# Optimization experiments

Measured on AMD Instinct MI355X. Metric: run time of the kernel, lower is better.

## Reference

```python
import jax, jax.numpy as jnp
import numpy as np

N = 100_000      # nodes
E = 1_600_000    # edges (avg degree 16)
D_IN = 128
D_OUT = 128
K = 64           # low-rank attention rank


def setup_inputs() -> dict:
    key = jax.random.key(0)
    ks = jax.random.split(key, 6)
    s = lambda d: 1.0 / np.sqrt(d)
    return {
        "x": jax.random.normal(ks[0], (N, D_IN), dtype=jnp.float32),
        "edge_index": jax.random.randint(ks[1], (2, E), 0, N, dtype=jnp.int32),
        "W_gcn": jax.random.normal(ks[2], (D_IN, D_OUT), dtype=jnp.float32) * s(D_IN),
        "b_gcn": jnp.zeros((D_OUT,), jnp.float32),
        "W_att": jax.random.normal(ks[3], (D_IN, 4 * K), dtype=jnp.float32) * s(D_IN),
        "b_att": jnp.zeros((4 * K,), jnp.float32),
        "W_red": jax.random.normal(ks[4], (D_OUT + 2 * K, D_OUT), dtype=jnp.float32) * s(D_OUT + 2 * K),
        "b_red": jnp.zeros((D_OUT,), jnp.float32),
    }


def _forward(x, W_gcn, b_gcn, W_att, b_att, W_red, b_red, edge_index):
    n = x.shape[0]
    # --- GCN conv (symmetric normalization, self-loops), dropout = identity (eval) ---
    loop = jnp.arange(n, dtype=edge_index.dtype)
    src = jnp.concatenate([edge_index[0], loop])
    dst = jnp.concatenate([edge_index[1], loop])
    deg = jax.ops.segment_sum(jnp.ones_like(dst, dtype=x.dtype), dst, num_segments=n)
    dinv = jax.lax.rsqrt(deg)                      # deg >= 1 due to self-loops
    norm = dinv[src] * dinv[dst]                   # [E+n]
    h = x @ W_gcn                                  # [n, D_OUT]
    agg = jax.ops.segment_sum(h[src] * norm[:, None], dst, num_segments=n) + b_gcn
    x_local = jax.nn.relu(agg)

    # --- Low-rank global attention (LRGA) ---
    t = jax.nn.relu(x @ W_att + b_att)             # [n, 4K]
    U, V, Z, T = jnp.split(t, 4, axis=1)           # each [n, K]
    # joint_normalize2: scalar 1/mean(U @ (V^T @ 1_n))
    D = 1.0 / jnp.mean(U @ (V.T @ jnp.ones((n, 1), x.dtype)))
    res = (U @ (V.T @ Z)) * D                      # [n, K]
    x_global = jnp.concatenate([res, T], axis=1)   # [n, 2K]

    # --- fuse + dim reduce ---
    return jnp.concatenate([x_local, x_global], axis=1) @ W_red + b_red


def reference(x, edge_index, W_gcn, b_gcn, W_att, b_att, W_red, b_red):
    return _forward(x, W_gcn, b_gcn, W_att, b_att, W_red, b_red, edge_index)
```

## Files before the change

### kernel.cpp

```cpp
#include <hip/hip_runtime.h>

#define DIN   128
#define DOUT  128
#define KR    64
#define TCOLS 256
#define WCOLS 384
#define P_RED 1024
#define PSTR  4224

typedef unsigned short ushort_t;
typedef __attribute__((ext_vector_type(8))) short bf16x8;
typedef __attribute__((ext_vector_type(4))) float f32x4;

__device__ __forceinline__ float bf2f(unsigned short u) {
  return __uint_as_float(((unsigned int)u) << 16);
}
__device__ __forceinline__ unsigned short f2bf(float f) {
  unsigned int b = __float_as_uint(f);
  b = b + 0x7FFFu + ((b >> 16) & 1u);
  return (unsigned short)(b >> 16);
}

__global__ __launch_bounds__(256) void k_init(int* __restrict__ degc, float* __restrict__ VtZ,
                                              float* __restrict__ colsum, int* __restrict__ bcur,
                                              int N) {
  int i = blockIdx.x * 256 + threadIdx.x;
  if (i < N) degc[i] = 1;
  if (i < 4096) VtZ[i] = 0.f;
  if (i < 128) colsum[i] = 0.f;
  if (i < 128) bcur[i] = 0;
}

__global__ __launch_bounds__(256) void k_deg(const int* __restrict__ ei, int* __restrict__ degc, int E) {
  int e = blockIdx.x * 256 + threadIdx.x;
  if (e < E) atomicAdd(&degc[ei[E + e]], 1);
}

__global__ __launch_bounds__(256) void k_split(const float* __restrict__ x,
                                               ushort_t* __restrict__ xhF, ushort_t* __restrict__ xloF,
                                               int N, int total_slots) {
  int gid = blockIdx.x * 256 + threadIdx.x;
  int stride = gridDim.x * 256;
  for (; gid < total_slots; gid += stride) {
    int f = gid >> 6, l = gid & 63;
    int r16 = f >> 2, s = f & 3;
    int row = r16 * 16 + (l & 15);
    int k = s * 32 + ((l >> 4) << 3);
    ushort4 h0, h1, l0, l1;
    if (row < N) {
      float4 a = *(const float4*)&x[(size_t)row * DIN + k];
      float4 b = *(const float4*)&x[(size_t)row * DIN + k + 4];
      h0.x = f2bf(a.x); h0.y = f2bf(a.y); h0.z = f2bf(a.z); h0.w = f2bf(a.w);
      h1.x = f2bf(b.x); h1.y = f2bf(b.y); h1.z = f2bf(b.z); h1.w = f2bf(b.w);
      l0.x = f2bf(a.x - bf2f(h0.x)); l0.y = f2bf(a.y - bf2f(h0.y));
      l0.z = f2bf(a.z - bf2f(h0.z)); l0.w = f2bf(a.w - bf2f(h0.w));
      l1.x = f2bf(b.x - bf2f(h1.x)); l1.y = f2bf(b.y - bf2f(h1.y));
      l1.z = f2bf(b.z - bf2f(h1.z)); l1.w = f2bf(b.w - bf2f(h1.w));
    } else {
      h0 = make_ushort4(0, 0, 0, 0); h1 = h0; l0 = h0; l1 = h0;
    }
    ((ushort4*)xhF)[gid * 2] = h0;
    ((ushort4*)xhF)[gid * 2 + 1] = h1;
    ((ushort4*)xloF)[gid * 2] = l0;
    ((ushort4*)xloF)[gid * 2 + 1] = l1;
  }
}

__global__ __launch_bounds__(256) void k_wprep(const float* __restrict__ Wg, const float* __restrict__ Wa,
                                               ushort_t* __restrict__ whF, ushort_t* __restrict__ wlF) {
  int g = blockIdx.x * 256 + threadIdx.x;
  int f = g >> 6, l = g & 63;
  int c16 = f >> 2, s = f & 3;
  int col = c16 * 16 + (l & 15);
  int k = s * 32 + ((l >> 4) << 3);
#pragma unroll
  for (int j = 0; j < 8; ++j) {
    float v = (col < DOUT) ? Wg[(size_t)(k + j) * DOUT + col]
                           : Wa[(size_t)(k + j) * TCOLS + (col - DOUT)];
    ushort_t h = f2bf(v);
    whF[(size_t)g * 8 + j] = h;
    wlF[(size_t)g * 8 + j] = f2bf(v - bf2f(h));
  }
}

__global__ __launch_bounds__(256) void k_scan1(const int* __restrict__ degc, int* __restrict__ offs,
                                               int* __restrict__ bsums, int N) {
  __shared__ int s[256];
  int tid = threadIdx.x;
  int base = blockIdx.x * 1024 + tid * 4;
  int c[4], e[4];
#pragma unroll
  for (int q = 0; q < 4; ++q) c[q] = (base + q < N) ? (degc[base + q] - 1) : 0;
  e[0] = 0; e[1] = c[0]; e[2] = e[1] + c[1]; e[3] = e[2] + c[2];
  int tsum = e[3] + c[3];
  s[tid] = tsum; __syncthreads();
  for (int off = 1; off < 256; off <<= 1) {
    int v = (tid >= off) ? s[tid - off] : 0;
    __syncthreads();
    s[tid] += v;
    __syncthreads();
  }
  int tb = s[tid] - tsum;
#pragma unroll
  for (int q = 0; q < 4; ++q) if (base + q < N) offs[base + q] = tb + e[q];
  if (tid == 255) bsums[blockIdx.x] = s[255];
}

__global__ __launch_bounds__(128) void k_scan2(const int* __restrict__ bsums, int* __restrict__ boff,
                                               int* __restrict__ offs, int NBLK, int N) {
  __shared__ int s[128];
  int tid = threadIdx.x;
  int v = (tid < NBLK) ? bsums[tid] : 0;
  s[tid] = v; __syncthreads();
  for (int off = 1; off < 128; off <<= 1) {
    int u = (tid >= off) ? s[tid - off] : 0;
    __syncthreads();
    s[tid] += u;
    __syncthreads();
  }
  boff[tid] = s[tid] - v;
  if (tid == 127) offs[N] = s[127];
}

__global__ __launch_bounds__(256) void k_scan3(int* __restrict__ offs, const int* __restrict__ boff,
                                               const int* __restrict__ degc, float* __restrict__ dinv,
                                               int* __restrict__ cursor, int N) {
  int i = blockIdx.x * 256 + threadIdx.x;
  if (i < N) {
    offs[i] += boff[i >> 10];
    dinv[i] = rsqrtf((float)degc[i]);
    cursor[i] = 0;
  }
}

__global__ __launch_bounds__(256) void k_bin(const int* __restrict__ ei, int* __restrict__ bcur,
                                             int2* __restrict__ buckets, int* __restrict__ cursor,
                                             const int* __restrict__ offs, const float* __restrict__ dinv,
                                             int2* __restrict__ csr, int E, int B, int CAP) {
  __shared__ int hist[128], pref[128], place[128], gbase[128];
  __shared__ int2 st[4096];
  int tid = threadIdx.x;
  int e0 = blockIdx.x * 4096;
  int nE = min(4096, E - e0);
  if (nE <= 0) return;

  if (tid < 128) { hist[tid] = 0; place[tid] = 0; }
  __syncthreads();

  int src[16], dst[16];
#pragma unroll
  for (int q = 0; q < 16; ++q) {
    int idx = tid + q * 256;
    if (idx < nE) {
      src[q] = ei[e0 + idx];
      dst[q] = ei[E + e0 + idx];
      atomicAdd(&hist[dst[q] >> 10], 1);
    }
  }
  __syncthreads();

  if (tid < 128) pref[tid] = hist[tid];
  __syncthreads();
  for (int off = 1; off < 128; off <<= 1) {
    int v = (tid < 128 && tid >= off) ? pref[tid - off] : 0;
    __syncthreads();
    if (tid < 128) pref[tid] += v;
    __syncthreads();
  }
  if (tid < 128) pref[tid] -= hist[tid];
  if (tid < B && hist[tid] > 0) gbase[tid] = atomicAdd(&bcur[tid], hist[tid]);
  __syncthreads();

#pragma unroll
  for (int q = 0; q < 16; ++q) {
    int idx = tid + q * 256;
    if (idx < nE) {
      int b = dst[q] >> 10;
      int p = pref[b] + atomicAdd(&place[b], 1);
      st[p] = make_int2(src[q], dst[q]);
    }
  }
  __syncthreads();

  for (int i = tid; i < nE; i += 256) {
    int2 q = st[i];
    int b = q.y >> 10;
    int gp = gbase[b] + (i - pref[b]);
    if (gp < CAP) {
      buckets[(size_t)b * CAP + gp] = q;
    } else {
      int pos = atomicAdd(&cursor[q.y], 1);
      int2 c;
      c.x = q.x;
      c.y = __float_as_int(dinv[q.x] * dinv[q.y]);
      csr[offs[q.y] + pos] = c;
    }
  }
}

__global__ __launch_bounds__(256) void k_scatter2(const int2* __restrict__ buckets,
                                                  const int* __restrict__ bcur,
                                                  int* __restrict__ cursor, const int* __restrict__ offs,
                                                  const float* __restrict__ dinv,
                                                  int2* __restrict__ csr, int CAP) {
  int b = blockIdx.x;
  int n = min(bcur[b], CAP);
  const int2* sp = &buckets[(size_t)b * CAP];
  for (int i = threadIdx.x; i < n; i += 256) {
    int2 q = sp[i];
    int pos = atomicAdd(&cursor[q.y], 1);
    int2 c;
    c.x = q.x;
    c.y = __float_as_int(dinv[q.x] * dinv[q.y]);
    csr[offs[q.y] + pos] = c;
  }
}

#define LOADK(S, AH, AL, BH, BL)                                              \
  {                                                                           \
    _Pragma("unroll") for (int m_ = 0; m_ < 4; ++m_) {                        \
      size_t fo_ = (((size_t)(r16b + m_) * 4 + (S)) * 64 + lane) * 8;         \
      AH[m_] = *(const bf16x8*)&xhF[fo_];                                     \
      AL[m_] = *(const bf16x8*)&xloF[fo_];                                    \
    }                                                                         \
    _Pragma("unroll") for (int n_ = 0; n_ < 4; ++n_) {                        \
      size_t fo_ = (((size_t)(c16b + n_) * 4 + (S)) * 64 + lane) * 8;         \
      BH[n_] = *(const bf16x8*)&whF[fo_];                                     \
      BL[n_] = *(const bf16x8*)&wlF[fo_];                                     \
    }                                                                         \
  }

__global__ __launch_bounds__(256) void k_gemm1_mfma(const ushort_t* __restrict__ xhF,
                                                    const ushort_t* __restrict__ xloF,
                                                    const ushort_t* __restrict__ whF,
                                                    const ushort_t* __restrict__ wlF,
                                                    const float* __restrict__ ba,
                                                    ushort_t* __restrict__ hs, ushort_t* __restrict__ t,
                                                    int N, int ntiles) {
  int bid = blockIdx.x;
  int g = bid / 24;
  int rem = bid - g * 24;
  int colblk = rem >> 3;
  int ytile = g * 8 + (rem & 7);
  if (ytile >= ntiles) return;

  int tid = threadIdx.x;
  int lane = tid & 63;
  int wave = tid >> 6;
  int wr = wave >> 1, wc = wave & 1;
  int rowbase = ytile * 128 + wr * 64;
  int gcb = colblk * 128 + wc * 64;
  int r16b = ytile * 8 + wr * 4;
  int c16b = colblk * 8 + wc * 4;
  int lr = lane & 15;
  int rq = (lane >> 4) * 4;

  f32x4 acc[4][4] = {};
  bf16x8 ah[2][4], al[2][4], bh[2][4], bl[2][4];

  LOADK(0, ah[0], al[0], bh[0], bl[0]);
#pragma unroll
  for (int s = 0; s < 4; ++s) {
    int cur = s & 1, nxt = cur ^ 1;
    if (s < 3) LOADK(s + 1, ah[nxt], al[nxt], bh[nxt], bl[nxt]);
#pragma unroll
    for (int m = 0; m < 4; ++m)
#pragma unroll
      for (int n = 0; n < 4; ++n) {
        acc[m][n] = __builtin_amdgcn_mfma_f32_16x16x32_bf16(ah[cur][m], bl[cur][n], acc[m][n], 0, 0, 0);
        acc[m][n] = __builtin_amdgcn_mfma_f32_16x16x32_bf16(al[cur][m], bh[cur][n], acc[m][n], 0, 0, 0);
        acc[m][n] = __builtin_amdgcn_mfma_f32_16x16x32_bf16(ah[cur][m], bh[cur][n], acc[m][n], 0, 0, 0);
      }
  }

  if (colblk == 0) {
#pragma unroll
    for (int m = 0; m < 4; ++m)
#pragma unroll
      for (int i = 0; i < 4; ++i) {
        int row = rowbase + m * 16 + rq + i;
        if (row < N) {
#pragma unroll
          for (int n = 0; n < 4; ++n)
            hs[(size_t)row * DOUT + gcb + n * 16 + lr] = f2bf(acc[m][n][i]);
        }
      }
  } else {
    float bav[4];
#pragma unroll
    for (int n = 0; n < 4; ++n) bav[n] = ba[gcb - DOUT + n * 16 + lr];
#pragma unroll
    for (int m = 0; m < 4; ++m)
#pragma unroll
      for (int i = 0; i < 4; ++i) {
        int row = rowbase + m * 16 + rq + i;
        if (row < N) {
#pragma unroll
          for (int n = 0; n < 4; ++n)
            t[(size_t)row * TCOLS + gcb - DOUT + n * 16 + lr] =
                f2bf(fmaxf(acc[m][n][i] + bav[n], 0.f));
        }
      }
  }
}

__global__ __launch_bounds__(256) void k_red(const ushort_t* __restrict__ t, float* __restrict__ part,
                                             int N) {
  __shared__ float csh[512];
  int tid = threadIdx.x;
  int lane = tid & 63;
  int w = tid >> 6;
  int lr = lane & 15;
  int lk = (lane >> 4) * 8;
  int vcol = 64 + w * 16 + lr;
  int col2 = lane * 2;

  f32x4 acc[4] = {};
  float cs0 = 0.f, cs1 = 0.f;
  int ntiles = (N + 31) >> 5;

  for (int tile = blockIdx.x; tile < ntiles; tile += gridDim.x) {
    int r0 = tile * 32;
    const ushort_t* base = &t[(size_t)r0 * TCOLS];
    bf16x8 a, b[4];
    if (r0 + 32 <= N) {
#pragma unroll
      for (int j = 0; j < 8; ++j)
        ((short*)&a)[j] = (short)base[(size_t)(lk + j) * TCOLS + vcol];
#pragma unroll
      for (int n = 0; n < 4; ++n)
#pragma unroll
        for (int j = 0; j < 8; ++j)
          ((short*)&b[n])[j] = (short)base[(size_t)(lk + j) * TCOLS + 128 + n * 16 + lr];
#pragma unroll
      for (int j = 0; j < 8; ++j) {
        ushort2 u = *(const ushort2*)&base[(size_t)(w * 8 + j) * TCOLS + col2];
        cs0 += bf2f(u.x); cs1 += bf2f(u.y);
      }
    } else {
#pragma unroll
      for (int j = 0; j < 8; ++j) {
        int r = r0 + lk + j;
        ((short*)&a)[j] = (r < N) ? (short)t[(size_t)r * TCOLS + vcol] : (short)0;
      }
#pragma unroll
      for (int n = 0; n < 4; ++n)
#pragma unroll
        for (int j = 0; j < 8; ++j) {
          int r = r0 + lk + j;
          ((short*)&b[n])[j] = (r < N) ? (short)t[(size_t)r * TCOLS + 128 + n * 16 + lr] : (short)0;
        }
#pragma unroll
      for (int j = 0; j < 8; ++j) {
        int r = r0 + w * 8 + j;
        if (r < N) {
          ushort2 u = *(const ushort2*)&t[(size_t)r * TCOLS + col2];
          cs0 += bf2f(u.x); cs1 += bf2f(u.y);
        }
      }
    }
#pragma unroll
    for (int n = 0; n < 4; ++n)
      acc[n] = __builtin_amdgcn_mfma_f32_16x16x32_bf16(a, b[n], acc[n], 0, 0, 0);
  }

  float* pb = &part[(size_t)blockIdx.x * PSTR];
  int rq = (lane >> 4) * 4;
#pragma unroll
  for (int n = 0; n < 4; ++n)
#pragma unroll
    for (int i = 0; i < 4; ++i)
      pb[(w * 16 + rq + i) * 64 + n * 16 + lr] = acc[n][i];

  csh[tid] = cs0;
  csh[256 + tid] = cs1;
  __syncthreads();
  if (w == 0) {
    float t0 = csh[lane] + csh[64 + lane] + csh[128 + lane] + csh[192 + lane];
    float t1 = csh[256 + lane] + csh[320 + lane] + csh[384 + lane] + csh[448 + lane];
    pb[4096 + col2] = t0;
    pb[4096 + col2 + 1] = t1;
  }
}

__global__ __launch_bounds__(256) void k_redsum(const float* __restrict__ part,
                                                float* __restrict__ VtZ, float* __restrict__ colsum) {
  __shared__ float s[256];
  int tid = threadIdx.x;
  int j = blockIdx.x * 64 + (tid & 63);
  int bc = tid >> 6;
  float a = 0.f;
#pragma unroll 4
  for (int b = bc; b < P_RED; b += 4) a += part[(size_t)b * PSTR + j];
  s[tid] = a;
  __syncthreads();
  if (bc == 0) {
    float v = s[tid] + s[tid + 64] + s[tid + 128] + s[tid + 192];
    if (j < 4096) VtZ[j] = v;
    else colsum[j - 4096] = v;
  }
}

__global__ __launch_bounds__(64) void k_d(const float* __restrict__ colsum, float* __restrict__ Dws, int N) {
  __shared__ float s[64];
  int k = threadIdx.x;
  s[k] = colsum[k] * colsum[64 + k];
  __syncthreads();
  for (int off = 32; off > 0; off >>= 1) {
    if (k < off) s[k] += s[k + off];
    __syncthreads();
  }
  if (k == 0) {
    float p = s[0];
    Dws[0] = (p != 0.f) ? ((float)N / p) : 0.f;
  }
}

__global__ __launch_bounds__(256) void k_prep(const float* __restrict__ VtZ,
                                              const float* __restrict__ Dws,
                                              const float* __restrict__ Wr,
                                              ushort_t* __restrict__ weffT) {
  int c = blockIdx.x;
  int k = threadIdx.x;
  float v;
  if (k < 128 || k >= 192) {
    v = Wr[(size_t)k * DOUT + c];
  } else {
    float Dv = Dws[0];
    int kk = k - 128;
    float acc = 0.f;
#pragma unroll 8
    for (int j = 0; j < 64; ++j)
      acc += VtZ[kk * 64 + j] * Wr[(size_t)(128 + j) * DOUT + c];
    v = acc * Dv;
  }
  weffT[(size_t)c * 256 + k] = f2bf(v);
}

__global__ __launch_bounds__(256) void k_out_mfma(const ushort_t* __restrict__ xl,
                                                  const ushort_t* __restrict__ t,
                                                  const ushort_t* __restrict__ weffT,
                                                  const float* __restrict__ br,
                                                  float* __restrict__ out, int N) {
  int tid = threadIdx.x;
  int lane = tid & 63;
  int wave = tid >> 6;
  int wr = wave >> 1, wc = wave & 1;
  int rowbase = blockIdx.x * 128 + wr * 64;
  int cbase = wc * 64;
  int lr = lane & 15;
  int lk = (lane >> 4) * 8;

  int rows[4];
#pragma unroll
  for (int m = 0; m < 4; ++m) {
    int r = rowbase + m * 16 + lr;
    rows[m] = (r < N) ? r : (N - 1);
  }

  f32x4 acc[4][4] = {};

#pragma unroll
  for (int s = 0; s < 8; ++s) {
    int k0 = s * 32 + lk;
    bf16x8 a[4], b[4];
#pragma unroll
    for (int m = 0; m < 4; ++m) {
      const ushort_t* ap;
      if (s < 4)      ap = &xl[(size_t)rows[m] * DOUT + k0];
      else if (s < 6) ap = &t[(size_t)rows[m] * TCOLS + (k0 - 128)];
      else            ap = &t[(size_t)rows[m] * TCOLS + k0];
      a[m] = *(const bf16x8*)ap;
    }
#pragma unroll
    for (int n = 0; n < 4; ++n) {
      int c = cbase + n * 16 + lr;
      b[n] = *(const bf16x8*)&weffT[(size_t)c * 256 + k0];
    }
#pragma unroll
    for (int m = 0; m < 4; ++m)
#pragma unroll
      for (int n = 0; n < 4; ++n)
        acc[m][n] = __builtin_amdgcn_mfma_f32_16x16x32_bf16(a[m], b[n], acc[m][n], 0, 0, 0);
  }

  float brv[4];
#pragma unroll
  for (int n = 0; n < 4; ++n) brv[n] = br[cbase + n * 16 + lr];

  int rq = (lane >> 4) * 4;
#pragma unroll
  for (int m = 0; m < 4; ++m) {
#pragma unroll
    for (int i = 0; i < 4; ++i) {
      int row = rowbase + m * 16 + rq + i;
      if (row < N) {
#pragma unroll
        for (int n = 0; n < 4; ++n)
          out[(size_t)row * DOUT + cbase + n * 16 + lr] = acc[m][n][i] + brv[n];
      }
    }
  }
}

__global__ __launch_bounds__(256) void k_aggn(const ushort_t* __restrict__ hs, const int2* __restrict__ csr,
                                              const int* __restrict__ offs, const float* __restrict__ dinv,
                                              const float* __restrict__ bg,
                                              ushort_t* __restrict__ xl, int N) {
  int node = blockIdx.x * 4 + (threadIdx.x >> 6);
  int lane = threadIdx.x & 63;
  if (node >= N) return;
  int c2 = 2 * lane;
  float dn = dinv[node];
  ushort2 u = *(const ushort2*)&hs[(size_t)node * DOUT + c2];
  float a0 = dn * dn * bf2f(u.x);
  float a1 = dn * dn * bf2f(u.y);
  int e = offs[node], e1 = offs[node + 1];
  for (; e + 4 <= e1; e += 4) {
    int2 q0 = csr[e], q1 = csr[e + 1], q2 = csr[e + 2], q3 = csr[e + 3];
    ushort2 r0 = *(const ushort2*)&hs[(size_t)q0.x * DOUT + c2];
    ushort2 r1 = *(const ushort2*)&hs[(size_t)q1.x * DOUT + c2];
    ushort2 r2 = *(const ushort2*)&hs[(size_t)q2.x * DOUT + c2];
    ushort2 r3 = *(const ushort2*)&hs[(size_t)q3.x * DOUT + c2];
    float n0 = __int_as_float(q0.y), n1 = __int_as_float(q1.y);
    float n2 = __int_as_float(q2.y), n3 = __int_as_float(q3.y);
    a0 += n0 * bf2f(r0.x) + n1 * bf2f(r1.x) + n2 * bf2f(r2.x) + n3 * bf2f(r3.x);
    a1 += n0 * bf2f(r0.y) + n1 * bf2f(r1.y) + n2 * bf2f(r2.y) + n3 * bf2f(r3.y);
  }
  for (; e < e1; ++e) {
    int2 q = csr[e];
    ushort2 r = *(const ushort2*)&hs[(size_t)q.x * DOUT + c2];
    float n0 = __int_as_float(q.y);
    a0 += n0 * bf2f(r.x);
    a1 += n0 * bf2f(r.y);
  }
  ushort2 o;
  o.x = f2bf(fmaxf(a0 + bg[c2], 0.f));
  o.y = f2bf(fmaxf(a1 + bg[c2 + 1], 0.f));
  *(ushort2*)&xl[(size_t)node * DOUT + c2] = o;
}

extern "C" void kernel_launch(void* const* d_in, const int* in_sizes, int n_in,
                              void* d_out, int out_size, void* d_ws, size_t ws_size,
                              hipStream_t stream) {
  const float* x  = (const float*)d_in[0];
  const int* ei   = (const int*)d_in[1];
  const float* Wg = (const float*)d_in[2];
  const float* bg = (const float*)d_in[3];
  const float* Wa = (const float*)d_in[4];
  const float* ba = (const float*)d_in[5];
  const float* Wr = (const float*)d_in[6];
  const float* br = (const float*)d_in[7];
  float* out = (float*)d_out;

  const int N = in_sizes[0] / DIN;
  const int E = in_sizes[1] / 2;

  const int NT128 = (N + 127) / 128;
  const int N16P = NT128 * 8;
  const int NFRAG_A = N16P * 4;
  const int B = (N + 1023) >> 10;
  const int CAP = ((E / (B > 0 ? B : 1)) * 3 / 2 + 255) & ~255;

  char* p = (char*)d_ws;
  auto alloc = [&](size_t bytes) {
    char* r = p;
    p += (bytes + 255) & ~(size_t)255;
    return r;
  };
  float* Dws    = (float*)alloc(256);
  float* colsum = (float*)alloc(128 * 4);
  float* VtZ    = (float*)alloc(4096 * 4);
  int*   bsums  = (int*)alloc(1024);
  int*   boff   = (int*)alloc(1024);
  int*   bcur   = (int*)alloc(1024);
  ushort_t* weffT = (ushort_t*)alloc(128 * 256 * 2);
  ushort_t* whF = (ushort_t*)alloc((size_t)24 * 4 * 512 * 2);
  ushort_t* wlF = (ushort_t*)alloc((size_t)24 * 4 * 512 * 2);
  float* part   = (float*)alloc((size_t)P_RED * PSTR * 4);
  int*   degc   = (int*)alloc((size_t)N * 4);
  float* dinv   = (float*)alloc((size_t)N * 4);
  int*   offs   = (int*)alloc((size_t)(N + 1) * 4);
  int*   cursor = (int*)alloc((size_t)N * 4);
  int2*  csr    = (int2*)alloc((size_t)E * 8);
  int2*  buckets= (int2*)alloc((size_t)B * CAP * 8);
  ushort_t* xhF = (ushort_t*)alloc((size_t)NFRAG_A * 512 * 2);
  ushort_t* xloF= (ushort_t*)alloc((size_t)NFRAG_A * 512 * 2);
  ushort_t* hs  = (ushort_t*)alloc((size_t)N * DOUT * 2);
  ushort_t* t   = (ushort_t*)alloc((size_t)N * TCOLS * 2);
  ushort_t* xl  = (ushort_t*)alloc((size_t)N * DOUT * 2);
  (void)ws_size; (void)n_in; (void)out_size;

  const int GN = (N + 255) / 256;
  const int GE = (E + 255) / 256;
  const int NBLK = (N + 1023) / 1024;
  const int G1 = ((NT128 + 7) / 8) * 24;
  const int GBIN = (E + 4095) / 4096;

  k_init<<<GN, 256, 0, stream>>>(degc, VtZ, colsum, bcur, N);
  k_deg<<<GE, 256, 0, stream>>>(ei, degc, E);
  k_split<<<2048, 256, 0, stream>>>(x, xhF, xloF, N, NFRAG_A * 64);
  k_wprep<<<24, 256, 0, stream>>>(Wg, Wa, whF, wlF);
  k_scan1<<<NBLK, 256, 0, stream>>>(degc, offs, bsums, N);
  k_scan2<<<1, 128, 0, stream>>>(bsums, boff, offs, NBLK, N);
  k_scan3<<<GN, 256, 0, stream>>>(offs, boff, degc, dinv, cursor, N);
  k_bin<<<GBIN, 256, 0, stream>>>(ei, bcur, buckets, cursor, offs, dinv, csr, E, B, CAP);
  k_scatter2<<<B, 256, 0, stream>>>(buckets, bcur, cursor, offs, dinv, csr, CAP);
  k_gemm1_mfma<<<G1, 256, 0, stream>>>(xhF, xloF, whF, wlF, ba, hs, t, N, NT128);
  k_red<<<P_RED, 256, 0, stream>>>(t, part, N);
  k_redsum<<<PSTR / 64, 256, 0, stream>>>(part, VtZ, colsum);
  k_d<<<1, 64, 0, stream>>>(colsum, Dws, N);
  k_prep<<<128, 256, 0, stream>>>(VtZ, Dws, Wr, weffT);
  k_aggn<<<(N + 3) / 4, 256, 0, stream>>>(hs, csr, offs, dinv, bg, xl, N);
  k_out_mfma<<<(N + 127) / 128, 256, 0, stream>>>(xl, t, weffT, br, out, N);
}
```

Before: 487.6 us.

## Split CSR scatter into quarter-bucket blocks with LDS-staged coalesced writes

The CSR build scatter now runs four blocks per 1024-node bucket. Each block handles 256 destination nodes, uses LDS cursors instead of global atomics, and stages its CSR slice in shared memory so the global write is coalesced. Bucket overflow edges are no longer scattered inside k_bin; they go to an overflow list that a new fixup kernel processes after the main scatter. This removes random global atomics and scattered writes, at the cost of each block reading the whole bucket four times and one extra launch.

```diff
diff --git a/kernel.cpp b/kernel.cpp
--- a/kernel.cpp
+++ b/kernel.cpp
@@ -7,6 +7,7 @@
 #define WCOLS 384
 #define P_RED 1024
 #define PSTR  4224
+#define STCAP 6144
 
 typedef unsigned short ushort_t;
 typedef __attribute__((ext_vector_type(8))) short bf16x8;
@@ -23,12 +24,13 @@
 
 __global__ __launch_bounds__(256) void k_init(int* __restrict__ degc, float* __restrict__ VtZ,
                                               float* __restrict__ colsum, int* __restrict__ bcur,
-                                              int N) {
+                                              int* __restrict__ ocnt, int N) {
   int i = blockIdx.x * 256 + threadIdx.x;
   if (i < N) degc[i] = 1;
   if (i < 4096) VtZ[i] = 0.f;
   if (i < 128) colsum[i] = 0.f;
   if (i < 128) bcur[i] = 0;
+  if (i == 0) ocnt[0] = 0;
 }
 
 __global__ __launch_bounds__(256) void k_deg(const int* __restrict__ ei, int* __restrict__ degc, int E) {
@@ -134,9 +136,9 @@
 }
 
 __global__ __launch_bounds__(256) void k_bin(const int* __restrict__ ei, int* __restrict__ bcur,
-                                             int2* __restrict__ buckets, int* __restrict__ cursor,
-                                             const int* __restrict__ offs, const float* __restrict__ dinv,
-                                             int2* __restrict__ csr, int E, int B, int CAP) {
+                                             int2* __restrict__ buckets,
+                                             int2* __restrict__ oflow, int* __restrict__ ocnt,
+                                             int E, int B, int CAP) {
   __shared__ int hist[128], pref[128], place[128], gbase[128];
   __shared__ int2 st[4096];
   int tid = threadIdx.x;
@@ -189,30 +191,61 @@
     if (gp < CAP) {
       buckets[(size_t)b * CAP + gp] = q;
     } else {
-      int pos = atomicAdd(&cursor[q.y], 1);
-      int2 c;
-      c.x = q.x;
-      c.y = __float_as_int(dinv[q.x] * dinv[q.y]);
-      csr[offs[q.y] + pos] = c;
+      int oi = atomicAdd(ocnt, 1);
+      oflow[oi] = q;
     }
   }
 }
 
 __global__ __launch_bounds__(256) void k_scatter2(const int2* __restrict__ buckets,
                                                   const int* __restrict__ bcur,
-                                                  int* __restrict__ cursor, const int* __restrict__ offs,
+                                                  const int* __restrict__ offs,
                                                   const float* __restrict__ dinv,
-                                                  int2* __restrict__ csr, int CAP) {
-  int b = blockIdx.x;
-  int n = min(bcur[b], CAP);
-  const int2* sp = &buckets[(size_t)b * CAP];
-  for (int i = threadIdx.x; i < n; i += 256) {
+                                                  int* __restrict__ cursor,
+                                                  int2* __restrict__ csr, int CAP, int N) {
+  __shared__ int lcur[256];
+  __shared__ int2 st[STCAP];
+  int cb = blockIdx.x >> 2;
+  int lo = cb * 1024 + (blockIdx.x & 3) * 256;
+  if (lo >= N) return;
+  int tid = threadIdx.x;
+  int nnode = min(256, N - lo);
+  int base = offs[lo];
+  int nb = offs[lo + nnode] - base;
+  if (tid < nnode) lcur[tid] = offs[lo + tid];
+  __syncthreads();
+  int avail = min(bcur[cb], CAP);
+  const int2* sp = &buckets[(size_t)cb * CAP];
+  bool staged = (nb <= STCAP);
+  int quarter = lo >> 8;
+  for (int i = tid; i < avail; i += 256) {
     int2 q = sp[i];
+    if ((q.y >> 8) != quarter) continue;
+    int p = atomicAdd(&lcur[q.y - lo], 1);
+    int2 c;
+    c.x = q.x;
+    c.y = __float_as_int(dinv[q.x] * dinv[q.y]);
+    if (staged) st[p - base] = c;
+    else        csr[p] = c;
+  }
+  __syncthreads();
+  if (staged) {
+    for (int i = tid; i < nb; i += 256) csr[base + i] = st[i];
+  }
+  if (tid < nnode) cursor[lo + tid] = lcur[tid];
+}
+
+__global__ __launch_bounds__(256) void k_fixup(const int2* __restrict__ oflow, const int* __restrict__ ocnt,
+                                               int* __restrict__ cursor, const float* __restrict__ dinv,
+                                               int2* __restrict__ csr) {
+  int n = ocnt[0];
+  for (int i = blockIdx.x * 256 + threadIdx.x; i < n; i += gridDim.x * 256) {
+    int2 q = oflow[i];
     int pos = atomicAdd(&cursor[q.y], 1);
     int2 c;
     c.x = q.x;
     c.y = __float_as_int(dinv[q.x] * dinv[q.y]);
-    csr[offs[q.y] + pos] = c;
+    csr[pos] = c;
   }
 }
 
@@ -574,6 +607,7 @@
   int*   bsums  = (int*)alloc(1024);
   int*   boff   = (int*)alloc(1024);
   int*   bcur   = (int*)alloc(1024);
+  int*   ocnt   = (int*)alloc(256);
   ushort_t* weffT = (ushort_t*)alloc(128 * 256 * 2);
   ushort_t* whF = (ushort_t*)alloc((size_t)24 * 4 * 512 * 2);
   ushort_t* wlF = (ushort_t*)alloc((size_t)24 * 4 * 512 * 2);
@@ -584,6 +618,7 @@
   int*   cursor = (int*)alloc((size_t)N * 4);
   int2*  csr    = (int2*)alloc((size_t)E * 8);
   int2*  buckets= (int2*)alloc((size_t)B * CAP * 8);
+  int2*  oflow  = (int2*)alloc((size_t)E * 8);
   ushort_t* xhF = (ushort_t*)alloc((size_t)NFRAG_A * 512 * 2);
   ushort_t* xloF= (ushort_t*)alloc((size_t)NFRAG_A * 512 * 2);
   ushort_t* hs  = (ushort_t*)alloc((size_t)N * DOUT * 2);
@@ -597,15 +632,16 @@
   const int G1 = ((NT128 + 7) / 8) * 24;
   const int GBIN = (E + 4095) / 4096;
 
-  k_init<<<GN, 256, 0, stream>>>(degc, VtZ, colsum, bcur, N);
+  k_init<<<GN, 256, 0, stream>>>(degc, VtZ, colsum, bcur, ocnt, N);
   k_deg<<<GE, 256, 0, stream>>>(ei, degc, E);
   k_split<<<2048, 256, 0, stream>>>(x, xhF, xloF, N, NFRAG_A * 64);
   k_wprep<<<24, 256, 0, stream>>>(Wg, Wa, whF, wlF);
   k_scan1<<<NBLK, 256, 0, stream>>>(degc, offs, bsums, N);
   k_scan2<<<1, 128, 0, stream>>>(bsums, boff, offs, NBLK, N);
   k_scan3<<<GN, 256, 0, stream>>>(offs, boff, degc, dinv, cursor, N);
-  k_bin<<<GBIN, 256, 0, stream>>>(ei, bcur, buckets, cursor, offs, dinv, csr, E, B, CAP);
-  k_scatter2<<<B, 256, 0, stream>>>(buckets, bcur, cursor, offs, dinv, csr, CAP);
+  k_bin<<<GBIN, 256, 0, stream>>>(ei, bcur, buckets, oflow, ocnt, E, B, CAP);
+  k_scatter2<<<B * 4, 256, 0, stream>>>(buckets, bcur, offs, dinv, cursor, csr, CAP, N);
+  k_fixup<<<32, 256, 0, stream>>>(oflow, ocnt, cursor, dinv, csr);
   k_gemm1_mfma<<<G1, 256, 0, stream>>>(xhF, xloF, whF, wlF, ba, hs, t, N, NT128);
   k_red<<<P_RED, 256, 0, stream>>>(t, part, N);
   k_redsum<<<PSTR / 64, 256, 0, stream>>>(part, VtZ, colsum);
```

New measurement: 450.8 us. 1.08x faster.
